# Kernel tuning notes

Hardware: AMD Instinct MI355X
Metric: run time of the kernel (lower is better)

The kernel has to match this reference:

```python
import jax, jax.numpy as jnp
import numpy as np

B, N, DIM = 4, 2048, 1024
HEADS, DIM_HEAD = 16, 64
INNER = HEADS * DIM_HEAD
SCALE = DIM_HEAD ** -0.5


def setup_inputs() -> dict:
    key = jax.random.key(0)
    k1, k2, k3 = jax.random.split(key, 3)
    x = jax.random.normal(k1, (B, N, DIM), dtype=jnp.float32)
    w_qkv = jax.random.normal(k2, (DIM, 3 * INNER), dtype=jnp.float32) * (DIM ** -0.5)
    w_out = jax.random.normal(k3, (INNER, DIM), dtype=jnp.float32) * (INNER ** -0.5)
    b_out = jnp.zeros((DIM,), dtype=jnp.float32)
    return {"x": x, "w_qkv": w_qkv, "w_out": w_out, "b_out": b_out}


def reference(x, w_qkv, w_out, b_out):
    # qkv projection: [B, N, 3*inner]
    qkv = jnp.einsum('bnd,de->bne', x, w_qkv)
    q, k, v = jnp.split(qkv, 3, axis=-1)
    # 'b n (h d) -> b h n d'
    split_heads = lambda t: t.reshape(B, N, HEADS, DIM_HEAD).transpose(0, 2, 1, 3)
    q, k, v = split_heads(q), split_heads(k), split_heads(v)
    dots = jnp.einsum('bhid,bhjd->bhij', q, k) * SCALE  # [B, H, N, N]
    attn = jax.nn.softmax(dots, axis=-1)
    out = jnp.einsum('bhij,bhjd->bhid', attn, v)
    # 'b h n d -> b n (h d)'
    out = out.transpose(0, 2, 1, 3).reshape(B, N, INNER)
    out = jnp.einsum('bne,ed->bnd', out, w_out) + b_out
    return out
```

## Files before the change

### kernel.cpp

```cpp
#include <hip/hip_runtime.h>
#include <hip/hip_bf16.h>
#include <stdint.h>

typedef float f32x4 __attribute__((ext_vector_type(4)));
typedef float f32x16 __attribute__((ext_vector_type(16)));
typedef short s16x8 __attribute__((ext_vector_type(8)));
typedef unsigned u32x4 __attribute__((ext_vector_type(4)));
typedef unsigned short us16;

#define LOG2E 1.44269504088896340736f

__device__ __forceinline__ us16 f2b(float f) {
  union { float f; unsigned u; } v; v.f = f;
  return (us16)((v.u + 0x7fffu + ((v.u >> 16) & 1u)) >> 16);
}

__device__ __forceinline__ unsigned cvtpk(float lo, float hi) {
  unsigned r;
  asm("v_cvt_pk_bf16_f32 %0, %1, %2" : "=v"(r) : "v"(lo), "v"(hi));
  return r;
}

__device__ __forceinline__ void plswap(unsigned& a, unsigned& b) {
  asm volatile("v_permlane32_swap_b32 %0, %1" : "+v"(a), "+v"(b));
}

__device__ __forceinline__ void gload16(const void* g, void* l) {
  __builtin_amdgcn_global_load_lds((__attribute__((address_space(1))) void*)g,
                                   (__attribute__((address_space(3))) void*)l,
                                   16, 0, 0);
}

#define MFMA16(acc, a, b) \
  (acc) = __builtin_amdgcn_mfma_f32_16x16x32_bf16((a), (b), (acc), 0, 0, 0)
#define MFMA32(acc, a, b) \
  (acc) = __builtin_amdgcn_mfma_f32_32x32x16_bf16((a), (b), (acc), 0, 0, 0)

__global__ void convx_kernel(const float* __restrict__ x, us16* __restrict__ xb) {
  const int idx = blockIdx.x * 256 + threadIdx.x;
  const float4 v = ((const float4*)x)[idx];
  ushort4 o;
  o.x = f2b(v.x); o.y = f2b(v.y); o.z = f2b(v.z); o.w = f2b(v.w);
  ((ushort4*)xb)[idx] = o;
}

__global__ void convw_kernel(const float* __restrict__ wqkv, const float* __restrict__ wout,
                             us16* __restrict__ wqkvT, us16* __restrict__ woutT) {
  __shared__ float tile[64][65];
  const int bid = blockIdx.x;
  const bool isq = bid < 768;
  const int j = isq ? bid : bid - 768;
  const int ntiles = isq ? 48 : 16;
  const int nt = j % ntiles, kt = j / ntiles;
  const int NN = isq ? 3072 : 1024;
  const float* W = isq ? wqkv : wout;
  us16* WT = isq ? wqkvT : woutT;
  const int n0 = nt * 64, k0 = kt * 64;
  const int t = threadIdx.x;
  const int tc = t & 63, tr = t >> 6;
#pragma unroll
  for (int p = 0; p < 16; ++p)
    tile[p * 4 + tr][tc] = W[(size_t)(k0 + p * 4 + tr) * NN + n0 + tc];
  __syncthreads();
#pragma unroll
  for (int p = 0; p < 16; ++p) {
    const int nl = p * 4 + tr;
    float v = tile[tc][nl];
    if (isq && (n0 + nl) < 1024) v *= 0.125f * LOG2E;
    WT[(size_t)(n0 + nl) * 1024 + k0 + tc] = f2b(v);
  }
}

template <int OUT_BF16>
__global__ __launch_bounds__(256, 2)
void gemm_bt(const us16* __restrict__ A, const us16* __restrict__ B,
             void* __restrict__ C, const float* __restrict__ bias, int N) {
  __shared__ us16 sm[2][2][128 * 64];
  const int t = threadIdx.x;
  const int l = t & 63;
  const int lr = l & 15, lh = l >> 4;
  const int w = t >> 6;
  const int wm = w >> 1, wn = w & 1;
  const int bm = blockIdx.x & 63;
  const int bn = blockIdx.x >> 6;
  const size_t m0 = (size_t)bm * 128, n0 = (size_t)bn * 128;

  f32x4 acc[4][4] = {};

  auto stage = [&](int buf, int kt) {
    const int k0 = kt << 6;
#pragma unroll
    for (int i = 0; i < 4; ++i) {
      const int e = i * 256 + t;
      const int r = e >> 3, c = (e & 7) << 3;
      gload16(A + (m0 + r) * 1024 + k0 + c, &sm[buf][0][e * 8]);
      gload16(B + (n0 + r) * 1024 + k0 + c, &sm[buf][1][e * 8]);
    }
  };

  stage(0, 0);
  __syncthreads();
  int cur = 0;
  for (int kt = 0; kt < 16; ++kt) {
    if (kt < 15) stage(cur ^ 1, kt + 1);
    const us16* sA = &sm[cur][0][0];
    const us16* sB = &sm[cur][1][0];
#pragma unroll
    for (int kk = 0; kk < 64; kk += 32) {
      s16x8 av[4], bv[4];
#pragma unroll
      for (int i = 0; i < 4; ++i)
        av[i] = *(const s16x8*)&sA[(wm * 64 + i * 16 + lr) * 64 + kk + lh * 8];
#pragma unroll
      for (int jj = 0; jj < 4; ++jj)
        bv[jj] = *(const s16x8*)&sB[(wn * 64 + jj * 16 + lr) * 64 + kk + lh * 8];
#pragma unroll
      for (int i = 0; i < 4; ++i)
#pragma unroll
        for (int jj = 0; jj < 4; ++jj)
          MFMA16(acc[i][jj], av[i], bv[jj]);
    }
    __syncthreads();
    cur ^= 1;
  }
#pragma unroll
  for (int i = 0; i < 4; ++i) {
    const size_t row0 = m0 + wm * 64 + i * 16 + lh * 4;
#pragma unroll
    for (int jj = 0; jj < 4; ++jj) {
      const size_t col = n0 + wn * 64 + jj * 16 + lr;
#pragma unroll
      for (int r = 0; r < 4; ++r) {
        const float v = acc[i][jj][r];
        if constexpr (OUT_BF16) {
          ((us16*)C)[(row0 + r) * N + col] = f2b(v);
        } else {
          ((float*)C)[(row0 + r) * N + col] = v + bias[col];
        }
      }
    }
  }
}

__global__ __launch_bounds__(512)
void attn_kernel(const us16* __restrict__ qkv, us16* __restrict__ attno) {
  __shared__ us16 Klds[2][64 * 64];
  __shared__ us16 Vt[2][64 * 64];
  const int tid = threadIdx.x;
  const int l31 = tid & 31;
  const int hi = (tid >> 5) & 1;
  const int w = tid >> 6;

  const int bid = blockIdx.x;
  const int bh = (bid & 7) * 8 + (bid >> 5);
  const int qt = (bid >> 3) & 3;
  const int b = bh >> 4, h = bh & 15;

  const size_t rowbase = (size_t)b * 2048;
  const int kcol = 1024 + h * 64, vcol = 2048 + h * 64;
  const size_t qrow0 = rowbase + qt * 512 + w * 64;

  s16x8 qa[4], qb[4];
  {
    const us16* qpa = qkv + (qrow0 + l31) * 3072 + h * 64 + hi * 8;
    const us16* qpb = qkv + (qrow0 + 32 + l31) * 3072 + h * 64 + hi * 8;
#pragma unroll
    for (int s = 0; s < 4; ++s) {
      qa[s] = *(const s16x8*)(qpa + s * 16);
      qb[s] = *(const s16x8*)(qpb + s * 16);
    }
  }

  const int tid4 = tid - 256;
  const int kvv = (tid & 31) * 2;
  const int vd0 = ((tid >> 5) & 7) * 8;
  auto stageK = [&](int buf, int kt2) {
#pragma unroll
    for (int i = 0; i < 2; ++i) {
      const int e = i * 256 + tid4;
      const int kv = e >> 3, sl = e & 7;
      gload16(qkv + (rowbase + (size_t)kt2 * 64 + kv) * 3072 + kcol + ((sl ^ (kv & 7)) << 3),
              &Klds[buf][e * 8]);
    }
  };
  auto vload = [&](int kt2, s16x8& a, s16x8& c) {
    const us16* vp = qkv + (rowbase + (size_t)kt2 * 64 + kvv) * 3072 + vcol + vd0;
    a = *(const s16x8*)vp;
    c = *(const s16x8*)(vp + 3072);
  };
  auto vwrite = [&](int buf, const s16x8 a, const s16x8 c) {
#pragma unroll
    for (int i = 0; i < 8; ++i) {
      const int row = vd0 + i;
      const unsigned pk = (unsigned)(us16)a[i] | ((unsigned)(us16)c[i] << 16);
      *(unsigned*)&Vt[buf][row * 64 + (kvv ^ ((row & 7) << 3))] = pk;
    }
  };

  f32x16 oA0 = {}, oA1 = {}, oB0 = {}, oB1 = {};
  float lsA = 0.0f, lsB = 0.0f;

  s16x8 vna, vnc;
  if (w < 4) { vload(0, vna, vnc); vwrite(0, vna, vnc); }
  else stageK(0, 0);
  __syncthreads();

  for (int kt = 0; kt < 32; ++kt) {
    const int cur = kt & 1;
    if (kt < 31) {
      if (w < 4) vload(kt + 1, vna, vnc);
      else stageK(cur ^ 1, kt + 1);
    }

    const us16* Kb = &Klds[cur][0];
    s16x8 kf0, kf1, kf2, kf3, kf4, kf5, kf6, kf7;
    {
      const int x7 = l31 & 7;
      kf0 = *(const s16x8*)&Kb[l31 * 64 + (((0 + hi) ^ x7) << 3)];
      kf1 = *(const s16x8*)&Kb[(32 + l31) * 64 + (((0 + hi) ^ x7) << 3)];
      kf2 = *(const s16x8*)&Kb[l31 * 64 + (((2 + hi) ^ x7) << 3)];
      kf3 = *(const s16x8*)&Kb[(32 + l31) * 64 + (((2 + hi) ^ x7) << 3)];
      kf4 = *(const s16x8*)&Kb[l31 * 64 + (((4 + hi) ^ x7) << 3)];
      kf5 = *(const s16x8*)&Kb[(32 + l31) * 64 + (((4 + hi) ^ x7) << 3)];
      kf6 = *(const s16x8*)&Kb[l31 * 64 + (((6 + hi) ^ x7) << 3)];
      kf7 = *(const s16x8*)&Kb[(32 + l31) * 64 + (((6 + hi) ^ x7) << 3)];
    }

    s16x8 paA[4], paB[4];
    {
      f32x16 st0 = {}, st1 = {};
      __builtin_amdgcn_s_setprio(1);
      MFMA32(st0, kf0, qa[0]); MFMA32(st1, kf1, qa[0]);
      MFMA32(st0, kf2, qa[1]); MFMA32(st1, kf3, qa[1]);
      MFMA32(st0, kf4, qa[2]); MFMA32(st1, kf5, qa[2]);
      MFMA32(st0, kf6, qa[3]); MFMA32(st1, kf7, qa[3]);
      __builtin_amdgcn_s_setprio(0);
      float ps = 0.0f;
#pragma unroll
      for (int r = 0; r < 16; ++r) {
        st0[r] = __builtin_amdgcn_exp2f(st0[r]);
        st1[r] = __builtin_amdgcn_exp2f(st1[r]);
        ps += st0[r] + st1[r];
      }
      lsA += ps;
#pragma unroll
      for (int half = 0; half < 2; ++half) {
        const f32x16& sp = half ? st1 : st0;
#pragma unroll
        for (int g = 0; g < 2; ++g) {
          unsigned a0 = cvtpk(sp[8 * g + 0], sp[8 * g + 1]);
          unsigned a1 = cvtpk(sp[8 * g + 2], sp[8 * g + 3]);
          unsigned b0 = cvtpk(sp[8 * g + 4], sp[8 * g + 5]);
          unsigned b1 = cvtpk(sp[8 * g + 6], sp[8 * g + 7]);
          plswap(a0, b0);
          plswap(a1, b1);
          union { u32x4 u; s16x8 s; } cv;
          cv.u = (u32x4){a0, a1, b0, b1};
          paA[2 * half + g] = cv.s;
        }
      }
    }
    {
      f32x16 st0 = {}, st1 = {};
      __builtin_amdgcn_s_setprio(1);
      MFMA32(st0, kf0, qb[0]); MFMA32(st1, kf1, qb[0]);
      MFMA32(st0, kf2, qb[1]); MFMA32(st1, kf3, qb[1]);
      MFMA32(st0, kf4, qb[2]); MFMA32(st1, kf5, qb[2]);
      MFMA32(st0, kf6, qb[3]); MFMA32(st1, kf7, qb[3]);
      __builtin_amdgcn_s_setprio(0);
      float ps = 0.0f;
#pragma unroll
      for (int r = 0; r < 16; ++r) {
        st0[r] = __builtin_amdgcn_exp2f(st0[r]);
        st1[r] = __builtin_amdgcn_exp2f(st1[r]);
        ps += st0[r] + st1[r];
      }
      lsB += ps;
#pragma unroll
      for (int half = 0; half < 2; ++half) {
        const f32x16& sp = half ? st1 : st0;
#pragma unroll
        for (int g = 0; g < 2; ++g) {
          unsigned a0 = cvtpk(sp[8 * g + 0], sp[8 * g + 1]);
          unsigned a1 = cvtpk(sp[8 * g + 2], sp[8 * g + 3]);
          unsigned b0 = cvtpk(sp[8 * g + 4], sp[8 * g + 5]);
          unsigned b1 = cvtpk(sp[8 * g + 6], sp[8 * g + 7]);
          plswap(a0, b0);
          plswap(a1, b1);
          union { u32x4 u; s16x8 s; } cv;
          cv.u = (u32x4){a0, a1, b0, b1};
          paB[2 * half + g] = cv.s;
        }
      }
    }

    const us16* Vb = &Vt[cur][0];
    __builtin_amdgcn_s_setprio(1);
#pragma unroll
    for (int ks = 0; ks < 4; ++ks) {
      const int sl = ((2 * ks + hi) ^ (l31 & 7)) << 3;
      const s16x8 vb0 = *(const s16x8*)&Vb[l31 * 64 + sl];
      const s16x8 vb1 = *(const s16x8*)&Vb[(32 + l31) * 64 + sl];
      MFMA32(oA0, paA[ks], vb0); MFMA32(oA1, paA[ks], vb1);
      MFMA32(oB0, paB[ks], vb0); MFMA32(oB1, paB[ks], vb1);
    }
    __builtin_amdgcn_s_setprio(0);

    if (kt < 31 && w < 4) vwrite(cur ^ 1, vna, vnc);
    __syncthreads();
  }

  const float lA = lsA + __shfl_xor(lsA, 32);
  const float lB = lsB + __shfl_xor(lsB, 32);
  const float liA = 1.0f / lA, liB = 1.0f / lB;
#pragma unroll
  for (int r = 0; r < 16; ++r) {
    const int q = (r & 3) + 8 * (r >> 2) + 4 * hi;
    const float fA = __shfl(liA, q);
    const float fB = __shfl(liB, q);
    const size_t rowA = qrow0 + q;
    const size_t rowB = qrow0 + 32 + q;
    attno[rowA * 1024 + h * 64 + l31] = f2b(oA0[r] * fA);
    attno[rowA * 1024 + h * 64 + 32 + l31] = f2b(oA1[r] * fA);
    attno[rowB * 1024 + h * 64 + l31] = f2b(oB0[r] * fB);
    attno[rowB * 1024 + h * 64 + 32 + l31] = f2b(oB1[r] * fB);
  }
}

extern "C" void kernel_launch(void* const* d_in, const int* in_sizes, int n_in,
                              void* d_out, int out_size, void* d_ws, size_t ws_size,
                              hipStream_t stream) {
  (void)in_sizes; (void)n_in; (void)out_size;
  const float* x     = (const float*)d_in[0];
  const float* w_qkv = (const float*)d_in[1];
  const float* w_out = (const float*)d_in[2];
  const float* b_out = (const float*)d_in[3];

  if (ws_size < 92274688u) return;
  char* ws = (char*)d_ws;
  us16* xb    = (us16*)(ws);
  us16* wqkvT = (us16*)(ws + 16777216);
  us16* woutT = (us16*)(ws + 23068672);
  us16* qkv   = (us16*)(ws + 25165824);
  us16* attno = (us16*)(ws + 75497472);

  convx_kernel<<<8192, 256, 0, stream>>>(x, xb);
  convw_kernel<<<1024, 256, 0, stream>>>(w_qkv, w_out, wqkvT, woutT);
  gemm_bt<1><<<1536, 256, 0, stream>>>(xb, wqkvT, (void*)qkv, nullptr, 3072);
  attn_kernel<<<256, 512, 0, stream>>>(qkv, attno);
  gemm_bt<0><<<512, 256, 0, stream>>>(attno, woutT, d_out, b_out, 1024);
}
```

Measured before the change: 181.3 us.

## Add 256x256 eight-wave QKV GEMM and compute softmax row sums via MFMA

Replaces the 128x128 QKV projection GEMM with a new 512-thread kernel that computes 256x256 output tiles. It uses split double-buffered LDS staging interleaved with MFMA phases, plus a block-index swizzle for L2 locality. The larger tiles give more data reuse per byte loaded. Separately, the attention kernel now accumulates softmax denominators with an extra MFMA against a ones vector, replacing the scalar adds and the cross-lane shuffles. That removes VALU work but adds matrix ops and accumulator registers, which raises register pressure.

```diff
diff --git a/kernel.cpp b/kernel.cpp
--- a/kernel.cpp
+++ b/kernel.cpp
@@ -71,6 +71,115 @@
   }
 }
 
+__global__ __launch_bounds__(512, 2)
+void gemm8p(const us16* __restrict__ A, const us16* __restrict__ Bm,
+            us16* __restrict__ C) {
+  __shared__ us16 As[2][2][128 * 64];
+  __shared__ us16 Bs[2][2][128 * 64];
+  const int t = threadIdx.x;
+  const int l = t & 63;
+  const int lr = l & 15, lh = l >> 4;
+  const int w = t >> 6;
+  const int wm = w >> 2, wn = w & 3;
+
+  const int bid = blockIdx.x;
+  const int swz = (bid & 7) * 48 + (bid >> 3);
+  const size_t m0 = (size_t)(swz & 31) * 256;
+  const size_t n0 = (size_t)(swz >> 5) * 256;
+
+  f32x4 acc[8][4] = {};
+
+  auto stage = [&](us16* dst, const us16* src, size_t rb, int kt2) {
+    if (kt2 < 16) {
+#pragma unroll
+      for (int i2 = 0; i2 < 2; ++i2) {
+        const int e = i2 * 512 + t;
+        const int row = e >> 3, slot = e & 7;
+        gload16(src + (rb + row) * 1024 + kt2 * 64 + ((slot ^ (row & 7)) << 3),
+                dst + e * 8);
+      }
+    }
+  };
+
+  stage(&As[0][0][0], A, m0, 0);        stage(&As[0][1][0], A, m0 + 128, 0);
+  stage(&Bs[0][0][0], Bm, n0, 0);       stage(&Bs[0][1][0], Bm, n0 + 128, 0);
+  stage(&Bs[1][0][0], Bm, n0, 1);       stage(&Bs[1][1][0], Bm, n0 + 128, 1);
+  asm volatile("s_waitcnt vmcnt(0)" ::: "memory");
+  asm volatile("s_barrier" ::: "memory");
+
+  const us16* aL = &As[0][wm][0];
+  const us16* aH = &As[1][wm][0];
+  const us16* bL = &Bs[0][wn >> 1][0];
+  const us16* bH = &Bs[1][wn >> 1][0];
+  const int brow0 = (wn & 1) * 64;
+
+  for (int it = 0; it < 8; ++it) {
+    const int T = 2 * it;
+    s16x8 bv[4][2];
+#pragma unroll
+    for (int p = 0; p < 8; ++p) {
+      const int q = p & 3;
+      const us16* ab = (p < 4) ? aL : aH;
+      const us16* bb = (p < 4) ? bL : bH;
+      s16x8 av[2][2];
+#pragma unroll
+      for (int j = 0; j < 2; ++j)
+#pragma unroll
+        for (int ks = 0; ks < 2; ++ks) {
+          const int row = (2 * q + j) * 16 + lr;
+          const int slot = (ks * 4 + lh) ^ (lr & 7);
+          av[j][ks] = *(const s16x8*)&ab[row * 64 + slot * 8];
+        }
+      if (q == 0) {
+#pragma unroll
+        for (int fc = 0; fc < 4; ++fc)
+#pragma unroll
+          for (int ks = 0; ks < 2; ++ks) {
+            const int row = brow0 + fc * 16 + lr;
+            const int slot = (ks * 4 + lh) ^ (lr & 7);
+            bv[fc][ks] = *(const s16x8*)&bb[row * 64 + slot * 8];
+          }
+      }
+      switch (p) {
+        case 0: stage(&As[1][0][0], A, m0, T + 1); break;
+        case 1: stage(&As[1][1][0], A, m0 + 128, T + 1); break;
+        case 2: stage(&Bs[0][0][0], Bm, n0, T + 2); break;
+        case 3: stage(&Bs[0][1][0], Bm, n0 + 128, T + 2); break;
+        case 4: stage(&As[0][0][0], A, m0, T + 2); break;
+        case 5: stage(&As[0][1][0], A, m0 + 128, T + 2); break;
+        case 6: stage(&Bs[1][0][0], Bm, n0, T + 3); break;
+        case 7: stage(&Bs[1][1][0], Bm, n0 + 128, T + 3); break;
+      }
+      asm volatile("s_barrier" ::: "memory");
+      __builtin_amdgcn_s_setprio(1);
+#pragma unroll
+      for (int fc = 0; fc < 4; ++fc)
+#pragma unroll
+        for (int j = 0; j < 2; ++j)
+#pragma unroll
+          for (int ks = 0; ks < 2; ++ks)
+            MFMA16(acc[2 * q + j][fc], av[j][ks], bv[fc][ks]);
+      __builtin_amdgcn_s_setprio(0);
+      if (p == 3 || p == 7) {
+        if (it == 7) { asm volatile("s_waitcnt vmcnt(0)" ::: "memory"); }
+        else         { asm volatile("s_waitcnt vmcnt(4)" ::: "memory"); }
+      }
+      asm volatile("s_barrier" ::: "memory");
+    }
+  }
+#pragma unroll
+  for (int fr = 0; fr < 8; ++fr) {
+    const size_t r0 = m0 + wm * 128 + fr * 16 + lh * 4;
+#pragma unroll
+    for (int fc = 0; fc < 4; ++fc) {
+      const size_t col = n0 + wn * 64 + fc * 16 + lr;
+#pragma unroll
+      for (int rg = 0; rg < 4; ++rg)
+        C[(r0 + rg) * 3072 + col] = f2b(acc[fr][fc][rg]);
+    }
+  }
+}
+
 template <int OUT_BF16>
 __global__ __launch_bounds__(256, 2)
 void gemm_bt(const us16* __restrict__ A, const us16* __restrict__ B,
@@ -171,6 +280,10 @@
     }
   }
 
+  s16x8 ones;
+#pragma unroll
+  for (int i = 0; i < 8; ++i) ones[i] = (short)0x3F80;
+
   const int tid4 = tid - 256;
   const int kvv = (tid & 31) * 2;
   const int vd0 = ((tid >> 5) & 7) * 8;
@@ -198,7 +311,7 @@
   };
 
   f32x16 oA0 = {}, oA1 = {}, oB0 = {}, oB1 = {};
-  float lsA = 0.0f, lsB = 0.0f;
+  f32x16 lsA = {}, lsB = {};
 
   s16x8 vna, vnc;
   if (w < 4) { vload(0, vna, vnc); vwrite(0, vna, vnc); }
@@ -235,14 +348,11 @@
       MFMA32(st0, kf4, qa[2]); MFMA32(st1, kf5, qa[2]);
       MFMA32(st0, kf6, qa[3]); MFMA32(st1, kf7, qa[3]);
       __builtin_amdgcn_s_setprio(0);
-      float ps = 0.0f;
 #pragma unroll
       for (int r = 0; r < 16; ++r) {
         st0[r] = __builtin_amdgcn_exp2f(st0[r]);
         st1[r] = __builtin_amdgcn_exp2f(st1[r]);
-        ps += st0[r] + st1[r];
-      }
-      lsA += ps;
+      }
 #pragma unroll
       for (int half = 0; half < 2; ++half) {
         const f32x16& sp = half ? st1 : st0;
@@ -268,14 +378,11 @@
       MFMA32(st0, kf4, qb[2]); MFMA32(st1, kf5, qb[2]);
       MFMA32(st0, kf6, qb[3]); MFMA32(st1, kf7, qb[3]);
       __builtin_amdgcn_s_setprio(0);
-      float ps = 0.0f;
 #pragma unroll
       for (int r = 0; r < 16; ++r) {
         st0[r] = __builtin_amdgcn_exp2f(st0[r]);
         st1[r] = __builtin_amdgcn_exp2f(st1[r]);
-        ps += st0[r] + st1[r];
-      }
-      lsB += ps;
+      }
 #pragma unroll
       for (int half = 0; half < 2; ++half) {
         const f32x16& sp = half ? st1 : st0;
@@ -303,6 +410,7 @@
       const s16x8 vb1 = *(const s16x8*)&Vb[(32 + l31) * 64 + sl];
       MFMA32(oA0, paA[ks], vb0); MFMA32(oA1, paA[ks], vb1);
       MFMA32(oB0, paB[ks], vb0); MFMA32(oB1, paB[ks], vb1);
+      MFMA32(lsA, paA[ks], ones); MFMA32(lsB, paB[ks], ones);
     }
     __builtin_amdgcn_s_setprio(0);
 
@@ -310,14 +418,11 @@
     __syncthreads();
   }
 
-  const float lA = lsA + __shfl_xor(lsA, 32);
-  const float lB = lsB + __shfl_xor(lsB, 32);
-  const float liA = 1.0f / lA, liB = 1.0f / lB;
 #pragma unroll
   for (int r = 0; r < 16; ++r) {
     const int q = (r & 3) + 8 * (r >> 2) + 4 * hi;
-    const float fA = __shfl(liA, q);
-    const float fB = __shfl(liB, q);
+    const float fA = 1.0f / lsA[r];
+    const float fB = 1.0f / lsB[r];
     const size_t rowA = qrow0 + q;
     const size_t rowB = qrow0 + 32 + q;
     attno[rowA * 1024 + h * 64 + l31] = f2b(oA0[r] * fA);
@@ -346,7 +451,7 @@
 
   convx_kernel<<<8192, 256, 0, stream>>>(x, xb);
   convw_kernel<<<1024, 256, 0, stream>>>(w_qkv, w_out, wqkvT, woutT);
-  gemm_bt<1><<<1536, 256, 0, stream>>>(xb, wqkvT, (void*)qkv, nullptr, 3072);
+  gemm8p<<<384, 512, 0, stream>>>(xb, wqkvT, qkv);
   attn_kernel<<<256, 512, 0, stream>>>(qkv, attno);
   gemm_bt<0><<<512, 256, 0, stream>>>(attno, woutT, d_out, b_out, 1024);
 }
```

After: 205.2 us. +13.2%, slower.
